# Kernel tuning notes

Hardware: AMD Instinct MI355X
Metric: run time of the kernel (lower is better)

Reference implementation:

```python
import jax, jax.numpy as jnp
import numpy as np
from jax import lax

B, C, H, W = 4, 256, 64, 64
C8 = C // 8


def _conv1x1(x, w, b):
    # x: (B,C,H,W), w: (O,C) -> (B,O,H,W)
    return jnp.einsum('bchw,oc->bohw', x, w) + b[None, :, None, None]


def setup_inputs() -> dict:
    key = jax.random.key(0)
    ks = jax.random.split(key, 9)
    s1 = 1.0 / np.sqrt(C)          # fan-in scale for 1x1 convs
    sf = 1.0 / np.sqrt(2 * C * 9)  # fan-in scale for 3x3 conv
    return {
        'front_x':     jax.random.normal(ks[0], (B, C, H, W), jnp.float32),
        'cross_x':     jax.random.normal(ks[1], (B, C, H, W), jnp.float32),
        'front_x_hat': jax.random.normal(ks[2], (B, C, H, W), jnp.float32),
        'Wq': jax.random.normal(ks[3], (C8, C), jnp.float32) * s1,
        'bq': jnp.zeros((C8,), jnp.float32),
        'Wk': jax.random.normal(ks[4], (C8, C), jnp.float32) * s1,
        'bk': jnp.zeros((C8,), jnp.float32),
        'Wv': jax.random.normal(ks[5], (C, C), jnp.float32) * s1,
        'bv': jnp.zeros((C,), jnp.float32),
        'Wf': jax.random.normal(ks[6], (C, 2 * C, 3, 3), jnp.float32) * sf,
        'bf': jnp.zeros((C,), jnp.float32),
    }


def reference(front_x, cross_x, front_x_hat, Wq, bq, Wk, bk, Wv, bv, Wf, bf):
    b, c, h, w = front_x.shape
    hw = h * w
    # projections -> (B, C/8, HW)
    q = _conv1x1(cross_x, Wq, bq).reshape(b, -1, hw)
    k = _conv1x1(front_x, Wk, bk).reshape(b, -1, hw)
    # energy[b,i,j] = <key_i, query_j>  (B, HW, HW)
    energy = jnp.einsum('bci,bcj->bij', k, q)
    front_star = jnp.max(energy, axis=1)     # (B, HW) best key score per query
    front_arg = jnp.argmax(energy, axis=1)   # (B, HW) best key index per query
    # value projection and hard gather of best-matching value per position
    v = _conv1x1(front_x_hat, Wv, bv).reshape(b, c, hw)
    T = jnp.take_along_axis(v, front_arg[:, None, :], axis=2).reshape(b, c, h, w)
    S = front_star.reshape(b, 1, h, w)
    cat = jnp.concatenate([front_x, T], axis=1)  # (B, 2C, H, W)
    res = lax.conv_general_dilated(
        cat, Wf, window_strides=(1, 1), padding='SAME',
        dimension_numbers=('NCHW', 'OIHW', 'NCHW')) + bf[None, :, None, None]
    return front_x + res * S
```

## Files before the change

kernel.cpp:

```cpp
#include <hip/hip_runtime.h>

#define Bn 4
#define Cn 256
#define C8 32
#define Hn 64
#define Wn 64
#define HWn 4096
#define PADR 80
#define ROWS (HWn + 2 * PADR)
#define MARGIN 6e-3f

typedef __bf16 bf16x8 __attribute__((ext_vector_type(8)));
typedef float floatx4 __attribute__((ext_vector_type(4)));
typedef unsigned short u16x8 __attribute__((ext_vector_type(8)));

__device__ __forceinline__ unsigned short f2bf(float f) {
  union { float f; unsigned int u; } c; c.f = f;
  unsigned int u = c.u;
  return (unsigned short)((u + 0x7FFFu + ((u >> 16) & 1u)) >> 16);
}
__device__ __forceinline__ float bf2f(unsigned short h) {
  union { unsigned int u; float f; } c; c.u = ((unsigned int)h) << 16;
  return c.f;
}
__device__ __forceinline__ void gl_lds16(const void* g, void* l) {
  __builtin_amdgcn_global_load_lds(
      (__attribute__((address_space(1))) void*)(uintptr_t)g,
      (__attribute__((address_space(3))) void*)(uintptr_t)l, 16, 0, 0);
}

__global__ void prep_w(const float* __restrict__ Wq, const float* __restrict__ Wk,
                       const float* __restrict__ Wv, const float* __restrict__ Wf,
                       float* __restrict__ Wqf, float* __restrict__ Wkf,
                       unsigned short* __restrict__ Wvb, unsigned short* __restrict__ Wfb,
                       int* __restrict__ cnt) {
  size_t t = (size_t)blockIdx.x * 256 + threadIdx.x;
  if (t == 0) cnt[0] = 0;
  if (t < 8192) {
    int o = (int)(t / 256), c = (int)(t % 256);
    Wqf[(size_t)c * 32 + o] = Wq[t];
    Wkf[(size_t)c * 32 + o] = Wk[t];
  }
  if (t < 65536) Wvb[t] = f2bf(Wv[t]);
  if (t < (size_t)9 * 256 * 512) {
    int tap = (int)(t / (256 * 512));
    int rem = (int)(t % (256 * 512));
    int o = rem / 512, ci = rem % 512;
    Wfb[t] = f2bf(Wf[((size_t)o * 512 + ci) * 9 + tap]);
  }
}

__global__ __launch_bounds__(1024) void proj_qk(
    const float* __restrict__ cross_x, const float* __restrict__ front_x,
    const float* __restrict__ Wqf, const float* __restrict__ bq,
    const float* __restrict__ Wkf, const float* __restrict__ bk,
    float* __restrict__ qf, float* __restrict__ kf,
    unsigned short* __restrict__ qhi, unsigned short* __restrict__ qlo,
    unsigned short* __restrict__ khi, unsigned short* __restrict__ klo) {
  int tid = threadIdx.x;
  int lane = tid & 63, wv = tid >> 6;
  int slice = wv & 3;
  int chunk = wv >> 2;
  int j = blockIdx.x * 64 + lane;
  int b = blockIdx.y;
  int z = blockIdx.z;
  const float* x = (z == 0) ? cross_x : front_x;
  const float* Wg = (z == 0) ? Wqf : Wkf;
  const float* bd = (z == 0) ? bq : bk;
  float* outp = (z == 0) ? qf : kf;
  unsigned short* hip_ = (z == 0) ? qhi : khi;
  unsigned short* lop_ = (z == 0) ? qlo : klo;
  int o0 = slice * 8;
  int c0 = chunk * 64;

  __shared__ __align__(16) float Wl[8192];
  __shared__ float part[3 * 4 * 8 * 64];

  for (int u = tid; u < 8192; u += 1024) Wl[u] = Wg[u];
  __syncthreads();

  const float* xb = x + (size_t)b * Cn * HWn + j;
  floatx4 a0 = (floatx4)0.0f, a1 = (floatx4)0.0f;
#pragma unroll 16
  for (int c = c0; c < c0 + 64; ++c) {
    float xv = xb[(size_t)c * HWn];
    floatx4 wa = *reinterpret_cast<const floatx4*>(&Wl[c * 32 + o0]);
    floatx4 wb = *reinterpret_cast<const floatx4*>(&Wl[c * 32 + o0 + 4]);
    a0 += wa * xv;
    a1 += wb * xv;
  }
  if (chunk > 0) {
    float* dst = &part[(((chunk - 1) * 4 + slice) * 8) * 64];
#pragma unroll
    for (int o = 0; o < 4; ++o) { dst[o * 64 + lane] = a0[o]; dst[(o + 4) * 64 + lane] = a1[o]; }
  }
  __syncthreads();
  if (chunk != 0) return;
#pragma unroll
  for (int q = 0; q < 3; ++q) {
    const float* src = &part[((q * 4 + slice) * 8) * 64];
#pragma unroll
    for (int o = 0; o < 4; ++o) { a0[o] += src[o * 64 + lane]; a1[o] += src[(o + 4) * 64 + lane]; }
  }
  float acc[8];
#pragma unroll
  for (int o = 0; o < 4; ++o) { acc[o] = a0[o] + bd[o0 + o]; acc[o + 4] = a1[o] + bd[o0 + 4 + o]; }

  float* op = outp + ((size_t)b * HWn + j) * C8 + o0;
  u16x8 hv, lv;
#pragma unroll
  for (int o = 0; o < 8; ++o) {
    op[o] = acc[o];
    unsigned short h = f2bf(acc[o]);
    hv[o] = h;
    lv[o] = f2bf(acc[o] - bf2f(h));
  }
  *reinterpret_cast<u16x8*>(hip_ + ((size_t)b * HWn + j) * C8 + o0) = hv;
  *reinterpret_cast<u16x8*>(lop_ + ((size_t)b * HWn + j) * C8 + o0) = lv;
}

__global__ __launch_bounds__(1024) void energy_approx(
    const unsigned short* __restrict__ khi, const unsigned short* __restrict__ klo,
    const unsigned short* __restrict__ qhi, const unsigned short* __restrict__ qlo,
    float* __restrict__ star, int* __restrict__ argb,
    int* __restrict__ cnt, int* __restrict__ list) {
  int b = blockIdx.y;
  int j0 = blockIdx.x * 32;
  int tid = threadIdx.x;
  int lane = tid & 63, wv = tid >> 6;
  int lm = lane & 15, lq = lane >> 4;

  __shared__ float bv1S[16][32];
  __shared__ int   bi1S[16][32];
  __shared__ float bv2S[16][32];

  bf16x8 qh[2], ql[2];
#pragma unroll
  for (int s = 0; s < 2; ++s) {
    int j = j0 + s * 16 + lm;
    qh[s] = *reinterpret_cast<const bf16x8*>(qhi + ((size_t)b * HWn + j) * 32 + lq * 8);
    ql[s] = *reinterpret_cast<const bf16x8*>(qlo + ((size_t)b * HWn + j) * 32 + lq * 8);
  }
  const unsigned short* kh_base = khi + (size_t)b * HWn * 32 + lq * 8;
  const unsigned short* kl_base = klo + (size_t)b * HWn * 32 + lq * 8;

  float b1[2], b2[2];
#pragma unroll
  for (int s = 0; s < 2; ++s) { b1[s] = -3.0e38f; b2[s] = -3.0e38f; }

  int ibase = wv * 256;
#pragma unroll 4
  for (int it = 0; it < 16; ++it) {
    int i0 = ibase + it * 16;
    bf16x8 ah = *reinterpret_cast<const bf16x8*>(kh_base + (size_t)(i0 + lm) * 32);
    bf16x8 al = *reinterpret_cast<const bf16x8*>(kl_base + (size_t)(i0 + lm) * 32);
#pragma unroll
    for (int s = 0; s < 2; ++s) {
      floatx4 acc = (floatx4)0.0f;
      acc = __builtin_amdgcn_mfma_f32_16x16x32_bf16(ah, qh[s], acc, 0, 0, 0);
      acc = __builtin_amdgcn_mfma_f32_16x16x32_bf16(ah, ql[s], acc, 0, 0, 0);
      acc = __builtin_amdgcn_mfma_f32_16x16x32_bf16(al, qh[s], acc, 0, 0, 0);
#pragma unroll
      for (int r = 0; r < 4; ++r) {
        unsigned code = (unsigned)(it * 4 + r);
        union { float f; unsigned u; } cv; cv.f = acc[r];
        cv.u = (cv.u & ~63u) | code;
        float vp = cv.f;
        b2[s] = __builtin_amdgcn_fmed3f(vp, b1[s], b2[s]);
        b1[s] = fmaxf(b1[s], vp);
      }
    }
  }
  int i1[2];
#pragma unroll
  for (int s = 0; s < 2; ++s) {
    union { float f; unsigned u; } cv; cv.f = b1[s];
    unsigned code = cv.u & 63u;
    i1[s] = ibase + (int)(code >> 2) * 16 + lq * 4 + (int)(code & 3u);
  }
#pragma unroll
  for (int s = 0; s < 2; ++s) {
#pragma unroll
    for (int m = 16; m <= 32; m <<= 1) {
      float ob1 = __shfl_xor(b1[s], m, 64);
      int oi1 = __shfl_xor(i1[s], m, 64);
      float ob2 = __shfl_xor(b2[s], m, 64);
      float c2;
      if (ob1 > b1[s] || (ob1 == b1[s] && oi1 < i1[s])) {
        c2 = fmaxf(b1[s], ob2);
        b1[s] = ob1; i1[s] = oi1;
      } else {
        c2 = fmaxf(ob1, b2[s]);
      }
      b2[s] = c2;
    }
    if (lq == 0) {
      bv1S[wv][s * 16 + lm] = b1[s];
      bi1S[wv][s * 16 + lm] = i1[s];
      bv2S[wv][s * 16 + lm] = b2[s];
    }
  }
  __syncthreads();
  if (tid < 32) {
    float B1 = bv1S[0][tid];
    int I1 = bi1S[0][tid];
    float B2 = bv2S[0][tid];
#pragma unroll
    for (int w = 1; w < 16; ++w) {
      float v1 = bv1S[w][tid];
      int ii = bi1S[w][tid];
      float v2 = bv2S[w][tid];
      if (v1 > B1) { B2 = fmaxf(B1, v2); B1 = v1; I1 = ii; }
      else B2 = fmaxf(B2, v1);
    }
    size_t o = (size_t)b * HWn + j0 + tid;
    union { float f; unsigned u; } cs; cs.f = B1;
    cs.u &= ~63u;
    star[o] = cs.f;
    argb[o] = I1;
    if (B1 - B2 < MARGIN) {
      int slot = atomicAdd(cnt, 1);
      list[slot] = (b << 12) | (j0 + (int)tid);
    }
  }
}

__global__ __launch_bounds__(256) void recheck(
    const float* __restrict__ qf, const float* __restrict__ kf,
    const int* __restrict__ cnt, const int* __restrict__ list,
    float* __restrict__ star, int* __restrict__ argb) {
  __shared__ double bvS[4];
  __shared__ int biS[4];
  int n = cnt[0];
  int tid = threadIdx.x;
  int lane = tid & 63, wv = tid >> 6;
  for (int idx = blockIdx.x; idx < n; idx += gridDim.x) {
    int e = list[idx];
    int b = e >> 12, j = e & 4095;
    const float* qp = qf + ((size_t)b * HWn + j) * 32;
    double qj[32];
#pragma unroll
    for (int o = 0; o < 32; ++o) qj[o] = (double)qp[o];
    double best = -1.0e300;
    int bi = 1 << 30;
    for (int i = tid; i < HWn; i += 256) {
      const float* kp = kf + ((size_t)b * HWn + i) * 32;
      double s = 0.0;
#pragma unroll
      for (int o = 0; o < 32; ++o) s += (double)kp[o] * qj[o];
      if (s > best) { best = s; bi = i; }
    }
#pragma unroll
    for (int m = 1; m < 64; m <<= 1) {
      double ob = __shfl_xor(best, m, 64);
      int oi = __shfl_xor(bi, m, 64);
      if (ob > best || (ob == best && oi < bi)) { best = ob; bi = oi; }
    }
    if (lane == 0) { bvS[wv] = best; biS[wv] = bi; }
    __syncthreads();
    if (tid == 0) {
#pragma unroll
      for (int w = 1; w < 4; ++w) {
        if (bvS[w] > best || (bvS[w] == best && biS[w] < bi)) {
          best = bvS[w]; bi = biS[w];
        }
      }
      star[(size_t)b * HWn + j] = (float)best;
      argb[(size_t)b * HWn + j] = bi;
    }
    __syncthreads();
  }
}

__global__ __launch_bounds__(256) void cat_fx(
    const float* __restrict__ fx, const float* __restrict__ fxh,
    unsigned short* __restrict__ catC, unsigned short* __restrict__ xht) {
  int j0 = blockIdx.x * 64;
  int ci0 = blockIdx.y * 64;
  int b = blockIdx.z >> 1;
  int which = blockIdx.z & 1;
  int tid = threadIdx.x;
  __shared__ unsigned short tile[64][66];

  const float* src = (which == 0) ? fx : fxh;
  for (int u = tid; u < 4096; u += 256) {
    int cl = u >> 6, hw_l = u & 63;
    tile[cl][hw_l] = f2bf(src[((size_t)(b * Cn + ci0 + cl)) * HWn + j0 + hw_l]);
  }
  __syncthreads();
  if (which == 0) {
    for (int u = tid; u < 4096; u += 256) {
      int hw_l = u >> 6, cl = u & 63;
      catC[((size_t)b * ROWS + PADR + j0 + hw_l) * 512 + ci0 + cl] = tile[cl][hw_l];
    }
  } else {
    for (int u = tid; u < 4096; u += 256) {
      int hw_l = u >> 6, cl = u & 63;
      xht[((size_t)b * HWn + j0 + hw_l) * 256 + ci0 + cl] = tile[cl][hw_l];
    }
  }
}

__global__ __launch_bounds__(256) void proj_v_mfma(
    const unsigned short* __restrict__ xht, const unsigned short* __restrict__ Wvb,
    const float* __restrict__ bv, unsigned short* __restrict__ vbf) {
  int m0 = blockIdx.x * 128;
  int o0 = blockIdx.y * 128;
  int b = blockIdx.z;
  int tid = threadIdx.x;
  int lane = tid & 63, wv = tid >> 6;
  int wm = wv >> 1, wn = wv & 1;
  int lm = lane & 15, lq = lane >> 4;

  union SMu {
    struct { unsigned short A[2][128 * 32]; unsigned short B[2][128 * 32]; } st;
    unsigned short TS[128 * 136];
  };
  __shared__ __align__(16) SMu sm;

  floatx4 acc[4][4];
#pragma unroll
  for (int im = 0; im < 4; ++im)
#pragma unroll
    for (int in = 0; in < 4; ++in) acc[im][in] = (floatx4)0.0f;

  const int srow = lane >> 2;
  const int soff = (((lane & 3) ^ ((lane >> 3) & 3)) * 8);
  const int sa = (lq ^ ((lm >> 1) & 3)) * 8;
  const unsigned short* ag = Wvb + (size_t)o0 * 256;
  const unsigned short* bg = xht + ((size_t)b * HWn + m0) * 256;

  auto STAGE = [&](unsigned short* Ab, unsigned short* Bb, int kc) {
#pragma unroll
    for (int i = 0; i < 2; ++i) {
      int r0 = wv * 32 + i * 16;
      gl_lds16(ag + ((size_t)(r0 + srow)) * 256 + kc + soff, &Ab[r0 * 32]);
      gl_lds16(bg + ((size_t)(r0 + srow)) * 256 + kc + soff, &Bb[r0 * 32]);
    }
  };
  auto COMPUTE = [&](const unsigned short* Ab, const unsigned short* Bb) {
    bf16x8 afr[4];
#pragma unroll
    for (int im = 0; im < 4; ++im)
      afr[im] = *reinterpret_cast<const bf16x8*>(
          &Ab[(wm * 64 + im * 16 + lm) * 32 + sa]);
#pragma unroll
    for (int in = 0; in < 4; ++in) {
      bf16x8 bfr = *reinterpret_cast<const bf16x8*>(
          &Bb[(wn * 64 + in * 16 + lm) * 32 + sa]);
#pragma unroll
      for (int im = 0; im < 4; ++im)
        acc[im][in] = __builtin_amdgcn_mfma_f32_16x16x32_bf16(
            afr[im], bfr, acc[im][in], 0, 0, 0);
    }
  };

  STAGE(sm.st.A[0], sm.st.B[0], 0);
  __syncthreads();
  for (int kci = 0; kci < 8; kci += 2) {
    if (kci < 7) STAGE(sm.st.A[1], sm.st.B[1], (kci + 1) * 32);
    COMPUTE(sm.st.A[0], sm.st.B[0]);
    __syncthreads();
    if (kci < 6) STAGE(sm.st.A[0], sm.st.B[0], (kci + 2) * 32);
    COMPUTE(sm.st.A[1], sm.st.B[1]);
    __syncthreads();
  }

#pragma unroll
  for (int in = 0; in < 4; ++in) {
    int pl = wn * 64 + in * 16 + lm;
#pragma unroll
    for (int im = 0; im < 4; ++im) {
#pragma unroll
      for (int r = 0; r < 4; ++r) {
        int ol = wm * 64 + im * 16 + lq * 4 + r;
        sm.TS[pl * 136 + ol] = f2bf(acc[im][in][r] + bv[o0 + ol]);
      }
    }
  }
  __syncthreads();
  for (int idx = tid; idx < 128 * 16; idx += 256) {
    int p = idx >> 4, ch = idx & 15;
    u16x8 val = *reinterpret_cast<const u16x8*>(&sm.TS[p * 136 + ch * 8]);
    *reinterpret_cast<u16x8*>(
        &vbf[((size_t)b * HWn + m0 + p) * 256 + o0 + ch * 8]) = val;
  }
}

__global__ __launch_bounds__(256) void gather_cat(
    const unsigned short* __restrict__ vbf, const int* __restrict__ argb,
    unsigned short* __restrict__ catC) {
  int b = blockIdx.y;
  int tid = threadIdx.x;
  if (blockIdx.x == 16) {
    for (int u = tid; u < 2 * PADR * 512; u += 256) {
      int r = u >> 9;
      int rr = (r < PADR) ? r : (HWn + r);
      catC[((size_t)b * ROWS + rr) * 512 + (u & 511)] = 0;
    }
    return;
  }
  __shared__ int ajS[256];
  int j0 = blockIdx.x * 256;
  ajS[tid] = argb[(size_t)b * HWn + j0 + tid];
  __syncthreads();
#pragma unroll 4
  for (int u = tid; u < 256 * 32; u += 256) {
    int pl = u >> 5, ch = u & 31;
    int aj = ajS[pl];
    u16x8 val = *reinterpret_cast<const u16x8*>(
        &vbf[((size_t)b * HWn + aj) * 256 + ch * 8]);
    *reinterpret_cast<u16x8*>(
        &catC[((size_t)b * ROWS + PADR + j0 + pl) * 512 + 256 + ch * 8]) = val;
  }
}

__global__ __launch_bounds__(256) void conv_mfma(
    const unsigned short* __restrict__ catC, const unsigned short* __restrict__ Wfb,
    unsigned short* __restrict__ Pg) {
  int m0 = blockIdx.x * 128;
  int o0 = blockIdx.y * 128;
  int bz = blockIdx.z;
  int b = bz / 3, g = bz % 3;
  int dy = g - 1;
  int tid = threadIdx.x;
  int lane = tid & 63;
  int wv = tid >> 6;
  int wm = wv >> 1, wn = wv & 1;
  int lm = lane & 15, lq = lane >> 4;
  const bool lane_first = (lm == 0);
  const bool lane_last = (lm == 15);

  __shared__ __align__(16) unsigned short AS[2][3 * 128 * 32];
  __shared__ __align__(16) unsigned short BS[2][144 * 32];

  floatx4 acc[4][4];
#pragma unroll
  for (int im = 0; im < 4; ++im)
#pragma unroll
    for (int in = 0; in < 4; ++in) acc[im][in] = (floatx4)0.0f;

  const int srow = lane >> 2;
  const int soff = (((lane & 3) ^ ((lane >> 3) & 3)) * 8);
  const int sa = (lq ^ ((lm >> 1) & 3)) * 8;
  const unsigned short* bg =
      catC + ((size_t)b * ROWS + PADR + m0 + dy * 64 - 1) * 512;
  const unsigned short* ag = Wfb + ((size_t)(g * 3) * 256 + o0) * 512;

  auto STAGE = [&](unsigned short* ASb, unsigned short* BSb, int kc) {
    if (wv < 3) {
      const unsigned short* at = ag + (size_t)wv * 256 * 512;
#pragma unroll
      for (int s = 0; s < 8; ++s)
        gl_lds16(at + ((size_t)(s * 16 + srow)) * 512 + kc + soff,
                 &ASb[(wv * 128 + s * 16) * 32]);
    } else {
#pragma unroll
      for (int s = 0; s < 9; ++s)
        gl_lds16(bg + ((size_t)(s * 16 + srow)) * 512 + kc + soff,
                 &BSb[(s * 16) * 32]);
    }
  };
  auto COMPUTE = [&](const unsigned short* ASb, const unsigned short* BSb) {
#pragma unroll
    for (int t = 0; t < 3; ++t) {
      bf16x8 afr[4];
#pragma unroll
      for (int im = 0; im < 4; ++im)
        afr[im] = *reinterpret_cast<const bf16x8*>(
            &ASb[(t * 128 + wm * 64 + im * 16 + lm) * 32 + sa]);
#pragma unroll
      for (int in = 0; in < 4; ++in) {
        int u = wn * 64 + in * 16 + lm + t;
        int sb = (lq ^ ((u >> 1) & 3)) * 8;
        u16x8 braw = *reinterpret_cast<const u16x8*>(&BSb[u * 32 + sb]);
        if ((t == 0 && in == 0 && lane_first) ||
            (t == 2 && in == 3 && lane_last))
          braw = (u16x8)(unsigned short)0;
        union { u16x8 u8; bf16x8 h; } cvt; cvt.u8 = braw;
#pragma unroll
        for (int im = 0; im < 4; ++im)
          acc[im][in] = __builtin_amdgcn_mfma_f32_16x16x32_bf16(
              afr[im], cvt.h, acc[im][in], 0, 0, 0);
      }
    }
  };

  STAGE(AS[0], BS[0], 0);
  __syncthreads();
  for (int kci = 0; kci < 16; kci += 2) {
    if (kci < 15) STAGE(AS[1], BS[1], (kci + 1) * 32);
    COMPUTE(AS[0], BS[0]);
    __syncthreads();
    if (kci < 14) STAGE(AS[0], BS[0], (kci + 2) * 32);
    COMPUTE(AS[1], BS[1]);
    __syncthreads();
  }

  unsigned short* P = Pg + ((size_t)(g * Bn + b) * Cn) * HWn;
#pragma unroll
  for (int in = 0; in < 4; ++in) {
    int p = m0 + wn * 64 + in * 16 + lm;
#pragma unroll
    for (int im = 0; im < 4; ++im) {
      int ob = o0 + wm * 64 + im * 16 + lq * 4;
#pragma unroll
      for (int r = 0; r < 4; ++r)
        P[(size_t)(ob + r) * HWn + p] = f2bf(acc[im][in][r]);
    }
  }
}

__global__ __launch_bounds__(256) void combine(
    const unsigned short* __restrict__ Pg, const float* __restrict__ fx,
    const float* __restrict__ bf, const float* __restrict__ star,
    float* __restrict__ out) {
  size_t e = ((size_t)blockIdx.x * 256 + threadIdx.x) * 8;
  int p = (int)(e & 4095);
  int bo = (int)(e >> 12);
  int o = bo & 255, b = bo >> 8;
  const size_t gs = (size_t)Bn * Cn * HWn;
  u16x8 q0 = *reinterpret_cast<const u16x8*>(Pg + e);
  u16x8 q1 = *reinterpret_cast<const u16x8*>(Pg + gs + e);
  u16x8 q2 = *reinterpret_cast<const u16x8*>(Pg + 2 * gs + e);
  float bias = bf[o];
  const float* sp = star + (size_t)b * HWn + p;
  const float* fp = fx + e;
  float* op = out + e;
#pragma unroll
  for (int h = 0; h < 2; ++h) {
    floatx4 s = *reinterpret_cast<const floatx4*>(sp + h * 4);
    floatx4 f = *reinterpret_cast<const floatx4*>(fp + h * 4);
    floatx4 r;
#pragma unroll
    for (int i = 0; i < 4; ++i) {
      int k = h * 4 + i;
      float a = bf2f(q0[k]) + bf2f(q1[k]) + bf2f(q2[k]);
      r[i] = f[i] + (a + bias) * s[i];
    }
    *reinterpret_cast<floatx4*>(op + h * 4) = r;
  }
}

extern "C" void kernel_launch(void* const* d_in, const int* in_sizes, int n_in,
                              void* d_out, int out_size, void* d_ws, size_t ws_size,
                              hipStream_t stream) {
  const float* front_x   = (const float*)d_in[0];
  const float* cross_x   = (const float*)d_in[1];
  const float* front_hat = (const float*)d_in[2];
  const float* Wq = (const float*)d_in[3];
  const float* bq = (const float*)d_in[4];
  const float* Wk = (const float*)d_in[5];
  const float* bk = (const float*)d_in[6];
  const float* Wv = (const float*)d_in[7];
  const float* bv = (const float*)d_in[8];
  const float* Wf = (const float*)d_in[9];
  const float* bf = (const float*)d_in[10];
  float* out = (float*)d_out;

  char* ws = (char*)d_ws;
  size_t off = 0;
  auto alloc = [&](size_t bytes) -> void* {
    void* p = (void*)(ws + off);
    off += (bytes + 255) & ~(size_t)255;
    return p;
  };
  float* Wqf = (float*)alloc(8192 * sizeof(float));
  float* Wkf = (float*)alloc(8192 * sizeof(float));
  unsigned short* Wvb = (unsigned short*)alloc(65536 * sizeof(unsigned short));
  unsigned short* Wfb = (unsigned short*)alloc((size_t)9 * 256 * 512 * sizeof(unsigned short));
  float* qf  = (float*)alloc((size_t)Bn * HWn * C8 * sizeof(float));
  float* kf  = (float*)alloc((size_t)Bn * HWn * C8 * sizeof(float));
  unsigned short* qhi = (unsigned short*)alloc((size_t)Bn * HWn * C8 * 2);
  unsigned short* qlo = (unsigned short*)alloc((size_t)Bn * HWn * C8 * 2);
  unsigned short* khi = (unsigned short*)alloc((size_t)Bn * HWn * C8 * 2);
  unsigned short* klo = (unsigned short*)alloc((size_t)Bn * HWn * C8 * 2);
  float*  star = (float*)alloc((size_t)Bn * HWn * sizeof(float));
  int*    argb = (int*)alloc((size_t)Bn * HWn * sizeof(int));
  int*    cnt  = (int*)alloc(256);
  int*    list = (int*)alloc((size_t)Bn * HWn * sizeof(int));
  unsigned short* xht = (unsigned short*)alloc((size_t)Bn * HWn * 256 * 2);
  unsigned short* vbf = (unsigned short*)alloc((size_t)Bn * HWn * 256 * 2);
  unsigned short* catC = (unsigned short*)alloc((size_t)Bn * ROWS * 512 * sizeof(unsigned short));
  unsigned short* Pg = (unsigned short*)alloc((size_t)3 * Bn * Cn * HWn * 2);

  prep_w<<<dim3((9 * 256 * 512 + 255) / 256), dim3(256), 0, stream>>>(
      Wq, Wk, Wv, Wf, Wqf, Wkf, Wvb, Wfb, cnt);

  proj_qk<<<dim3(HWn / 64, Bn, 2), dim3(1024), 0, stream>>>(
      cross_x, front_x, Wqf, bq, Wkf, bk, qf, kf, qhi, qlo, khi, klo);

  energy_approx<<<dim3(HWn / 32, Bn), dim3(1024), 0, stream>>>(
      khi, klo, qhi, qlo, star, argb, cnt, list);

  recheck<<<dim3(256), dim3(256), 0, stream>>>(qf, kf, cnt, list, star, argb);

  cat_fx<<<dim3(HWn / 64, Cn / 64, Bn * 2), dim3(256), 0, stream>>>(
      front_x, front_hat, catC, xht);

  proj_v_mfma<<<dim3(HWn / 128, Cn / 128, Bn), dim3(256), 0, stream>>>(
      xht, Wvb, bv, vbf);

  gather_cat<<<dim3(HWn / 256 + 1, Bn), dim3(256), 0, stream>>>(vbf, argb, catC);

  conv_mfma<<<dim3(HWn / 128, Cn / 128, Bn * 3), dim3(256), 0, stream>>>(
      catC, Wfb, Pg);

  combine<<<dim3((Bn * Cn * HWn / 8) / 256), dim3(256), 0, stream>>>(
      Pg, front_x, bf, star, out);
}
```

Baseline: 240.6 us.

## Fuse 3x3 conv row-groups and epilogue into single conv kernel

```diff
diff --git a/kernel.cpp b/kernel.cpp
--- a/kernel.cpp
+++ b/kernel.cpp
@@ -417,47 +417,48 @@
 
 __global__ __launch_bounds__(256) void conv_mfma(
     const unsigned short* __restrict__ catC, const unsigned short* __restrict__ Wfb,
-    unsigned short* __restrict__ Pg) {
-  int m0 = blockIdx.x * 128;
+    const float* __restrict__ fx, const float* __restrict__ bfc,
+    const float* __restrict__ star, float* __restrict__ out) {
+  int m0 = blockIdx.x * 64;
   int o0 = blockIdx.y * 128;
-  int bz = blockIdx.z;
-  int b = bz / 3, g = bz % 3;
-  int dy = g - 1;
+  int b = blockIdx.z;
   int tid = threadIdx.x;
   int lane = tid & 63;
   int wv = tid >> 6;
   int wm = wv >> 1, wn = wv & 1;
   int lm = lane & 15, lq = lane >> 4;
-  const bool lane_first = (lm == 0);
-  const bool lane_last = (lm == 15);
+  const bool edge_first = (wn == 0) && (lm == 0);
+  const bool edge_last  = (wn == 1) && (lm == 15);
 
   __shared__ __align__(16) unsigned short AS[2][3 * 128 * 32];
-  __shared__ __align__(16) unsigned short BS[2][144 * 32];
-
-  floatx4 acc[4][4];
+  __shared__ __align__(16) unsigned short BS[2][80 * 32];
+
+  floatx4 acc[4][2];
 #pragma unroll
   for (int im = 0; im < 4; ++im)
 #pragma unroll
-    for (int in = 0; in < 4; ++in) acc[im][in] = (floatx4)0.0f;
+    for (int in = 0; in < 2; ++in) acc[im][in] = (floatx4)0.0f;
 
   const int srow = lane >> 2;
   const int soff = (((lane & 3) ^ ((lane >> 3) & 3)) * 8);
   const int sa = (lq ^ ((lm >> 1) & 3)) * 8;
-  const unsigned short* bg =
-      catC + ((size_t)b * ROWS + PADR + m0 + dy * 64 - 1) * 512;
-  const unsigned short* ag = Wfb + ((size_t)(g * 3) * 256 + o0) * 512;
-
-  auto STAGE = [&](unsigned short* ASb, unsigned short* BSb, int kc) {
+  const unsigned short* catb = catC + ((size_t)b * ROWS + PADR + m0 - 65) * 512;
+  const unsigned short* wfo = Wfb + (size_t)o0 * 512;
+
+  auto STAGE = [&](unsigned short* ASb, unsigned short* BSb, int step) {
+    int g = step >> 4;
+    int kc = (step & 15) * 32;
     if (wv < 3) {
-      const unsigned short* at = ag + (size_t)wv * 256 * 512;
+      const unsigned short* at = wfo + (size_t)(g * 3 + wv) * 256 * 512;
 #pragma unroll
       for (int s = 0; s < 8; ++s)
         gl_lds16(at + ((size_t)(s * 16 + srow)) * 512 + kc + soff,
                  &ASb[(wv * 128 + s * 16) * 32]);
     } else {
-#pragma unroll
-      for (int s = 0; s < 9; ++s)
-        gl_lds16(bg + ((size_t)(s * 16 + srow)) * 512 + kc + soff,
+      const unsigned short* bt = catb + (size_t)(g * 64) * 512;
+#pragma unroll
+      for (int s = 0; s < 5; ++s)
+        gl_lds16(bt + ((size_t)(s * 16 + srow)) * 512 + kc + soff,
                  &BSb[(s * 16) * 32]);
     }
   };
@@ -470,12 +471,12 @@
         afr[im] = *reinterpret_cast<const bf16x8*>(
             &ASb[(t * 128 + wm * 64 + im * 16 + lm) * 32 + sa]);
 #pragma unroll
-      for (int in = 0; in < 4; ++in) {
-        int u = wn * 64 + in * 16 + lm + t;
+      for (int in = 0; in < 2; ++in) {
+        int u = wn * 32 + in * 16 + lm + t;
         int sb = (lq ^ ((u >> 1) & 3)) * 8;
         u16x8 braw = *reinterpret_cast<const u16x8*>(&BSb[u * 32 + sb]);
-        if ((t == 0 && in == 0 && lane_first) ||
-            (t == 2 && in == 3 && lane_last))
+        if ((t == 0 && in == 0 && edge_first) ||
+            (t == 2 && in == 1 && edge_last))
           braw = (u16x8)(unsigned short)0;
         union { u16x8 u8; bf16x8 h; } cvt; cvt.u8 = braw;
 #pragma unroll
@@ -488,57 +489,28 @@
 
   STAGE(AS[0], BS[0], 0);
   __syncthreads();
-  for (int kci = 0; kci < 16; kci += 2) {
-    if (kci < 15) STAGE(AS[1], BS[1], (kci + 1) * 32);
+  for (int st = 0; st < 48; st += 2) {
+    if (st < 47) STAGE(AS[1], BS[1], st + 1);
     COMPUTE(AS[0], BS[0]);
     __syncthreads();
-    if (kci < 14) STAGE(AS[0], BS[0], (kci + 2) * 32);
+    if (st < 46) STAGE(AS[0], BS[0], st + 2);
     COMPUTE(AS[1], BS[1]);
     __syncthreads();
   }
 
-  unsigned short* P = Pg + ((size_t)(g * Bn + b) * Cn) * HWn;
-#pragma unroll
-  for (int in = 0; in < 4; ++in) {
-    int p = m0 + wn * 64 + in * 16 + lm;
+#pragma unroll
+  for (int in = 0; in < 2; ++in) {
+    int p = m0 + wn * 32 + in * 16 + lm;
+    float s = star[(size_t)b * HWn + p];
 #pragma unroll
     for (int im = 0; im < 4; ++im) {
       int ob = o0 + wm * 64 + im * 16 + lq * 4;
 #pragma unroll
-      for (int r = 0; r < 4; ++r)
-        P[(size_t)(ob + r) * HWn + p] = f2bf(acc[im][in][r]);
-    }
-  }
-}
-
-__global__ __launch_bounds__(256) void combine(
-    const unsigned short* __restrict__ Pg, const float* __restrict__ fx,
-    const float* __restrict__ bf, const float* __restrict__ star,
-    float* __restrict__ out) {
-  size_t e = ((size_t)blockIdx.x * 256 + threadIdx.x) * 8;
-  int p = (int)(e & 4095);
-  int bo = (int)(e >> 12);
-  int o = bo & 255, b = bo >> 8;
-  const size_t gs = (size_t)Bn * Cn * HWn;
-  u16x8 q0 = *reinterpret_cast<const u16x8*>(Pg + e);
-  u16x8 q1 = *reinterpret_cast<const u16x8*>(Pg + gs + e);
-  u16x8 q2 = *reinterpret_cast<const u16x8*>(Pg + 2 * gs + e);
-  float bias = bf[o];
-  const float* sp = star + (size_t)b * HWn + p;
-  const float* fp = fx + e;
-  float* op = out + e;
-#pragma unroll
-  for (int h = 0; h < 2; ++h) {
-    floatx4 s = *reinterpret_cast<const floatx4*>(sp + h * 4);
-    floatx4 f = *reinterpret_cast<const floatx4*>(fp + h * 4);
-    floatx4 r;
-#pragma unroll
-    for (int i = 0; i < 4; ++i) {
-      int k = h * 4 + i;
-      float a = bf2f(q0[k]) + bf2f(q1[k]) + bf2f(q2[k]);
-      r[i] = f[i] + (a + bias) * s[i];
-    }
-    *reinterpret_cast<floatx4*>(op + h * 4) = r;
+      for (int r = 0; r < 4; ++r) {
+        size_t idx = ((size_t)(b * Cn + ob + r)) * HWn + p;
+        out[idx] = fx[idx] + (acc[im][in][r] + bfc[ob + r]) * s;
+      }
+    }
   }
 }
 
@@ -582,7 +554,6 @@
   unsigned short* xht = (unsigned short*)alloc((size_t)Bn * HWn * 256 * 2);
   unsigned short* vbf = (unsigned short*)alloc((size_t)Bn * HWn * 256 * 2);
   unsigned short* catC = (unsigned short*)alloc((size_t)Bn * ROWS * 512 * sizeof(unsigned short));
-  unsigned short* Pg = (unsigned short*)alloc((size_t)3 * Bn * Cn * HWn * 2);
 
   prep_w<<<dim3((9 * 256 * 512 + 255) / 256), dim3(256), 0, stream>>>(
       Wq, Wk, Wv, Wf, Wqf, Wkf, Wvb, Wfb, cnt);
@@ -603,9 +574,6 @@
 
   gather_cat<<<dim3(HWn / 256 + 1, Bn), dim3(256), 0, stream>>>(vbf, argb, catC);
 
-  conv_mfma<<<dim3(HWn / 128, Cn / 128, Bn * 3), dim3(256), 0, stream>>>(
-      catC, Wfb, Pg);
-
-  combine<<<dim3((Bn * Cn * HWn / 8) / 256), dim3(256), 0, stream>>>(
-      Pg, front_x, bf, star, out);
-}
+  conv_mfma<<<dim3(HWn / 64, Cn / 128, Bn), dim3(256), 0, stream>>>(
+      catC, Wfb, front_x, bf, star, out);
+}
```

Measured after the change: 244.4 us. About the same (+1.6%).

## Vectorize cat transpose kernel and overlap V-projection loads with fine-grained vmcnt waits

Applied to the files above, without the earlier changes.

```diff
diff --git a/kernel.cpp b/kernel.cpp
--- a/kernel.cpp
+++ b/kernel.cpp
@@ -283,21 +283,27 @@
   __shared__ unsigned short tile[64][66];
 
   const float* src = (which == 0) ? fx : fxh;
-  for (int u = tid; u < 4096; u += 256) {
-    int cl = u >> 6, hw_l = u & 63;
-    tile[cl][hw_l] = f2bf(src[((size_t)(b * Cn + ci0 + cl)) * HWn + j0 + hw_l]);
+#pragma unroll
+  for (int u = tid; u < 1024; u += 256) {
+    int cl = u >> 4, h4 = (u & 15) * 4;
+    floatx4 v = *reinterpret_cast<const floatx4*>(
+        &src[((size_t)(b * Cn + ci0 + cl)) * HWn + j0 + h4]);
+#pragma unroll
+    for (int k = 0; k < 4; ++k) tile[cl][h4 + k] = f2bf(v[k]);
   }
   __syncthreads();
-  if (which == 0) {
-    for (int u = tid; u < 4096; u += 256) {
-      int hw_l = u >> 6, cl = u & 63;
-      catC[((size_t)b * ROWS + PADR + j0 + hw_l) * 512 + ci0 + cl] = tile[cl][hw_l];
-    }
-  } else {
-    for (int u = tid; u < 4096; u += 256) {
-      int hw_l = u >> 6, cl = u & 63;
-      xht[((size_t)b * HWn + j0 + hw_l) * 256 + ci0 + cl] = tile[cl][hw_l];
-    }
+#pragma unroll
+  for (int u = tid; u < 512; u += 256) {
+    int oct = u & 7, hw_l = u >> 3;
+    u16x8 val;
+#pragma unroll
+    for (int k = 0; k < 8; ++k) val[k] = tile[oct * 8 + k][hw_l];
+    if (which == 0)
+      *reinterpret_cast<u16x8*>(
+          &catC[((size_t)b * ROWS + PADR + j0 + hw_l) * 512 + ci0 + oct * 8]) = val;
+    else
+      *reinterpret_cast<u16x8*>(
+          &xht[((size_t)b * HWn + j0 + hw_l) * 256 + ci0 + oct * 8]) = val;
   }
 }
 
@@ -330,24 +336,24 @@
   const unsigned short* ag = Wvb + (size_t)o0 * 256;
   const unsigned short* bg = xht + ((size_t)b * HWn + m0) * 256;
 
-  auto STAGE = [&](unsigned short* Ab, unsigned short* Bb, int kc) {
+  auto STAGE = [&](int buf, int kc) {
 #pragma unroll
     for (int i = 0; i < 2; ++i) {
       int r0 = wv * 32 + i * 16;
-      gl_lds16(ag + ((size_t)(r0 + srow)) * 256 + kc + soff, &Ab[r0 * 32]);
-      gl_lds16(bg + ((size_t)(r0 + srow)) * 256 + kc + soff, &Bb[r0 * 32]);
+      gl_lds16(ag + ((size_t)(r0 + srow)) * 256 + kc + soff, &sm.st.A[buf][r0 * 32]);
+      gl_lds16(bg + ((size_t)(r0 + srow)) * 256 + kc + soff, &sm.st.B[buf][r0 * 32]);
     }
   };
-  auto COMPUTE = [&](const unsigned short* Ab, const unsigned short* Bb) {
+  auto COMPUTE = [&](int buf) {
     bf16x8 afr[4];
 #pragma unroll
     for (int im = 0; im < 4; ++im)
       afr[im] = *reinterpret_cast<const bf16x8*>(
-          &Ab[(wm * 64 + im * 16 + lm) * 32 + sa]);
+          &sm.st.A[buf][(wm * 64 + im * 16 + lm) * 32 + sa]);
 #pragma unroll
     for (int in = 0; in < 4; ++in) {
       bf16x8 bfr = *reinterpret_cast<const bf16x8*>(
-          &Bb[(wn * 64 + in * 16 + lm) * 32 + sa]);
+          &sm.st.B[buf][(wn * 64 + in * 16 + lm) * 32 + sa]);
 #pragma unroll
       for (int im = 0; im < 4; ++im)
         acc[im][in] = __builtin_amdgcn_mfma_f32_16x16x32_bf16(
@@ -355,16 +361,21 @@
     }
   };
 
-  STAGE(sm.st.A[0], sm.st.B[0], 0);
-  __syncthreads();
-  for (int kci = 0; kci < 8; kci += 2) {
-    if (kci < 7) STAGE(sm.st.A[1], sm.st.B[1], (kci + 1) * 32);
-    COMPUTE(sm.st.A[0], sm.st.B[0]);
-    __syncthreads();
-    if (kci < 6) STAGE(sm.st.A[0], sm.st.B[0], (kci + 2) * 32);
-    COMPUTE(sm.st.A[1], sm.st.B[1]);
-    __syncthreads();
-  }
+  STAGE(0, 0);
+#pragma unroll 2
+  for (int st = 0; st < 8; ++st) {
+    __builtin_amdgcn_s_barrier();
+    if (st < 7) {
+      STAGE((st + 1) & 1, (st + 1) * 32);
+      asm volatile("s_waitcnt vmcnt(4)" ::: "memory");
+    } else {
+      asm volatile("s_waitcnt vmcnt(0)" ::: "memory");
+    }
+    __builtin_amdgcn_s_barrier();
+    __builtin_amdgcn_sched_barrier(0);
+    COMPUTE(st & 1);
+  }
+  __builtin_amdgcn_s_barrier();
 
 #pragma unroll
   for (int in = 0; in < 4; ++in) {
```

New measurement: 240.9 us. About the same (+0.1%).
